# Optimization experiments

Hardware: AMD Instinct MI355X
Metric: run time of the kernel (lower is better)

The kernel has to match this reference:

```python
import jax, jax.numpy as jnp
import numpy as np

NUM_EMBEDDINGS = 1024
EMBEDDING_DIM = 256
COMMITMENT_COST = 0.25


def setup_inputs() -> dict:
    key = jax.random.key(0)
    kz, kc = jax.random.split(key)
    z = jax.random.normal(kz, (32, 32, 32, EMBEDDING_DIM), dtype=jnp.float32)
    # torch init: uniform(-1/K, 1/K)
    codebook = jax.random.uniform(
        kc, (NUM_EMBEDDINGS, EMBEDDING_DIM), dtype=jnp.float32,
        minval=-1.0 / NUM_EMBEDDINGS, maxval=1.0 / NUM_EMBEDDINGS)
    return {"z": z, "codebook": codebook}


def reference(z, codebook):
    K, D = codebook.shape
    zf = z.reshape(-1, D)                                   # [N, D]
    # squared L2 distances via expansion: ||z||^2 + ||e||^2 - 2 z.e
    distances = (jnp.sum(zf * zf, axis=1, keepdims=True)
                 + jnp.sum(codebook * codebook, axis=1)
                 - 2.0 * jnp.matmul(zf, codebook.T))        # [N, K]
    idx = jnp.argmin(distances, axis=1)                     # [N]
    encodings = jax.nn.one_hot(idx, K, dtype=z.dtype)       # [N, K]
    quantized = jnp.matmul(encodings, codebook).reshape(z.shape)
    e_latent_loss = jnp.mean((jax.lax.stop_gradient(quantized) - z) ** 2)
    q_latent_loss = jnp.mean((quantized - jax.lax.stop_gradient(z)) ** 2)
    loss = q_latent_loss + COMMITMENT_COST * e_latent_loss
    quantized_st = z + jax.lax.stop_gradient(quantized - z)  # straight-through
    return quantized_st, loss, encodings
```

## Files before the change

### kernel.cpp

```cpp
#include <hip/hip_runtime.h>

#define N_ROWS 32768
#define DIM 256
#define K_CODES 1024
#define OUT_QUANT 8388608

__device__ __forceinline__ float pw128sq(const float* __restrict__ x) {
  float r[8];
#pragma unroll
  for (int j = 0; j < 8; ++j) r[j] = __fmul_rn(x[j], x[j]);
#pragma unroll
  for (int i = 8; i < 128; i += 8) {
#pragma unroll
    for (int j = 0; j < 8; ++j) r[j] = __fadd_rn(r[j], __fmul_rn(x[i + j], x[i + j]));
  }
  return __fadd_rn(__fadd_rn(__fadd_rn(r[0], r[1]), __fadd_rn(r[2], r[3])),
                   __fadd_rn(__fadd_rn(r[4], r[5]), __fadd_rn(r[6], r[7])));
}

__global__ __launch_bounds__(256) void row_norms(const float* __restrict__ z,
                                                 float* __restrict__ rn) {
  int r = blockIdx.x * 256 + threadIdx.x;
  if (r < N_ROWS)
    rn[r] = __fadd_rn(pw128sq(z + (size_t)r * DIM), pw128sq(z + (size_t)r * DIM + 128));
}

__global__ __launch_bounds__(256) void code_norms(const float* __restrict__ cb,
                                                  float* __restrict__ cn) {
  int k = blockIdx.x * 256 + threadIdx.x;
  if (k < K_CODES)
    cn[k] = __fadd_rn(pw128sq(cb + (size_t)k * DIM), pw128sq(cb + (size_t)k * DIM + 128));
}

__global__ __launch_bounds__(256) void gemm_argmin(
    const float* __restrict__ z, const float* __restrict__ cb,
    const float* __restrict__ rn, const float* __restrict__ cn,
    unsigned long long* __restrict__ keys) {
  __shared__ float As[16][132];
  __shared__ float Bs[16][132];
  __shared__ unsigned long long red[128];

  const int bm = blockIdx.x >> 3;
  const int bn = blockIdx.x & 7;
  const int row0 = bm * 128, col0 = bn * 128;
  const int tid = threadIdx.x;
  const int tx = tid & 15, ty = tid >> 4;
  const int lrow = tid >> 2;
  const int lc4 = (tid & 3) << 2;

  if (tid < 128) red[tid] = ~0ull;

  float acc[8][8];
#pragma unroll
  for (int i = 0; i < 8; ++i)
#pragma unroll
    for (int j = 0; j < 8; ++j) acc[i][j] = 0.f;

  for (int kk = 0; kk < DIM; kk += 16) {
    float4 a0 = *(const float4*)(z + (size_t)(row0 + lrow) * DIM + kk + lc4);
    float4 a1 = *(const float4*)(z + (size_t)(row0 + lrow + 64) * DIM + kk + lc4);
    float4 b0 = *(const float4*)(cb + (size_t)(col0 + lrow) * DIM + kk + lc4);
    float4 b1 = *(const float4*)(cb + (size_t)(col0 + lrow + 64) * DIM + kk + lc4);
    __syncthreads();
    As[lc4 + 0][lrow] = a0.x; As[lc4 + 1][lrow] = a0.y;
    As[lc4 + 2][lrow] = a0.z; As[lc4 + 3][lrow] = a0.w;
    As[lc4 + 0][lrow + 64] = a1.x; As[lc4 + 1][lrow + 64] = a1.y;
    As[lc4 + 2][lrow + 64] = a1.z; As[lc4 + 3][lrow + 64] = a1.w;
    Bs[lc4 + 0][lrow] = b0.x; Bs[lc4 + 1][lrow] = b0.y;
    Bs[lc4 + 2][lrow] = b0.z; Bs[lc4 + 3][lrow] = b0.w;
    Bs[lc4 + 0][lrow + 64] = b1.x; Bs[lc4 + 1][lrow + 64] = b1.y;
    Bs[lc4 + 2][lrow + 64] = b1.z; Bs[lc4 + 3][lrow + 64] = b1.w;
    __syncthreads();
#pragma unroll
    for (int k = 0; k < 16; ++k) {
      float av[8], bv[8];
      *(float4*)&av[0] = *(const float4*)&As[k][ty * 8];
      *(float4*)&av[4] = *(const float4*)&As[k][ty * 8 + 4];
      *(float4*)&bv[0] = *(const float4*)&Bs[k][tx * 4];
      *(float4*)&bv[4] = *(const float4*)&Bs[k][tx * 4 + 64];
#pragma unroll
      for (int i = 0; i < 8; ++i)
#pragma unroll
        for (int j = 0; j < 8; ++j) acc[i][j] = fmaf(av[i], bv[j], acc[i][j]);
    }
  }

#pragma unroll
  for (int i = 0; i < 8; ++i) {
    const int m = ty * 8 + i;
    const float a = rn[row0 + m];
    unsigned long long best = ~0ull;
#pragma unroll
    for (int j = 0; j < 8; ++j) {
      const int c = col0 + ((j < 4) ? (tx * 4 + j) : (64 + tx * 4 + (j - 4)));
      const float d = __fsub_rn(__fadd_rn(a, cn[c]), 2.0f * acc[i][j]);
      unsigned int b = __float_as_uint(d);
      b = (b & 0x80000000u) ? ~b : (b | 0x80000000u);
      const unsigned long long key = ((unsigned long long)b << 32) | (unsigned int)c;
      if (key < best) best = key;
    }
    atomicMin(&red[m], best);
  }
  __syncthreads();
  if (tid < 128) atomicMin(&keys[row0 + tid], red[tid]);
}

__global__ __launch_bounds__(256) void quantize_out(
    const float* __restrict__ z, const float* __restrict__ cb,
    const unsigned long long* __restrict__ keys,
    float* __restrict__ out, float* __restrict__ lossp) {
  __shared__ float ls[4];
  const int wid = threadIdx.x >> 6, lane = threadIdx.x & 63;
  const int row = blockIdx.x * 4 + wid;
  const int idx = (int)(keys[row] & 0xffffffffull);
  const float4 zv = *(const float4*)(z + (size_t)row * DIM + lane * 4);
  const float4 qv = *(const float4*)(cb + (size_t)idx * DIM + lane * 4);
  const float dx = __fsub_rn(qv.x, zv.x);
  const float dy = __fsub_rn(qv.y, zv.y);
  const float dzz = __fsub_rn(qv.z, zv.z);
  const float dw = __fsub_rn(qv.w, zv.w);
  float4 ov;
  ov.x = __fadd_rn(zv.x, dx); ov.y = __fadd_rn(zv.y, dy);
  ov.z = __fadd_rn(zv.z, dzz); ov.w = __fadd_rn(zv.w, dw);
  *(float4*)(out + (size_t)row * DIM + lane * 4) = ov;
  float s = dx * dx + dy * dy + dzz * dzz + dw * dw;
#pragma unroll
  for (int o = 32; o > 0; o >>= 1) s += __shfl_down(s, o);
  if (lane == 0) ls[wid] = s;
  __syncthreads();
  if (threadIdx.x == 0) lossp[blockIdx.x] = ls[0] + ls[1] + ls[2] + ls[3];
  if (lane == 0) out[(size_t)OUT_QUANT + 1 + (size_t)row * K_CODES + idx] = 1.0f;
}

__global__ __launch_bounds__(256) void loss_final(const float* __restrict__ lossp,
                                                  float* __restrict__ out) {
  __shared__ float sm[256];
  float v = 0.f;
  for (int i = threadIdx.x; i < 8192; i += 256) v += lossp[i];
  sm[threadIdx.x] = v;
  __syncthreads();
  for (int s = 128; s > 0; s >>= 1) {
    if (threadIdx.x < s) sm[threadIdx.x] += sm[threadIdx.x + s];
    __syncthreads();
  }
  if (threadIdx.x == 0) out[OUT_QUANT] = sm[0] * (1.25f / 8388608.0f);
}

extern "C" void kernel_launch(void* const* d_in, const int* in_sizes, int n_in,
                              void* d_out, int out_size, void* d_ws, size_t ws_size,
                              hipStream_t stream) {
  const float* z = (const float*)d_in[0];
  const float* cb = (const float*)d_in[1];
  float* out = (float*)d_out;

  unsigned long long* keys = (unsigned long long*)d_ws;
  float* rn = (float*)((char*)d_ws + (size_t)N_ROWS * 8);
  float* cn = rn + N_ROWS;
  float* lossp = cn + K_CODES;

  hipMemsetAsync(out + OUT_QUANT, 0, (size_t)(1 + (size_t)N_ROWS * K_CODES) * sizeof(float), stream);
  hipMemsetAsync(keys, 0xFF, (size_t)N_ROWS * 8, stream);

  row_norms<<<N_ROWS / 256, 256, 0, stream>>>(z, rn);
  code_norms<<<K_CODES / 256, 256, 0, stream>>>(cb, cn);
  gemm_argmin<<<2048, 256, 0, stream>>>(z, cb, rn, cn, keys);
  quantize_out<<<N_ROWS / 4, 256, 0, stream>>>(z, cb, keys, out, lossp);
  loss_final<<<1, 256, 0, stream>>>(lossp, out);
}
```

Measured before the change: 429.3 us.

## Use split-bf16 MFMA for distance GEMM and write one-hot rows directly

```diff
diff --git a/kernel.cpp b/kernel.cpp
--- a/kernel.cpp
+++ b/kernel.cpp
@@ -4,6 +4,10 @@
 #define DIM 256
 #define K_CODES 1024
 #define OUT_QUANT 8388608
+
+typedef unsigned long long ull;
+typedef __attribute__((ext_vector_type(8))) short bf16x8;
+typedef __attribute__((ext_vector_type(4))) float f32x4;
 
 __device__ __forceinline__ float pw128sq(const float* __restrict__ x) {
   float r[8];
@@ -32,83 +36,149 @@
     cn[k] = __fadd_rn(pw128sq(cb + (size_t)k * DIM), pw128sq(cb + (size_t)k * DIM + 128));
 }
 
-__global__ __launch_bounds__(256) void gemm_argmin(
-    const float* __restrict__ z, const float* __restrict__ cb,
+__device__ __forceinline__ void split3(float x, unsigned short& h, unsigned short& m,
+                                       unsigned short& l) {
+  unsigned int u = __float_as_uint(x);
+  unsigned int hb = u & 0xFFFF0000u;
+  h = (unsigned short)(hb >> 16);
+  float r1 = __fsub_rn(x, __uint_as_float(hb));
+  unsigned int mb = __float_as_uint(r1) & 0xFFFF0000u;
+  m = (unsigned short)(mb >> 16);
+  float r2 = __fsub_rn(r1, __uint_as_float(mb));
+  unsigned int u2 = __float_as_uint(r2);
+  unsigned int rounded = u2 + 0x7FFFu + ((u2 >> 16) & 1u);
+  l = (unsigned short)(rounded >> 16);
+}
+
+__global__ __launch_bounds__(256) void split_z(const float* __restrict__ z,
+                                               unsigned short* __restrict__ zh,
+                                               unsigned short* __restrict__ zm,
+                                               unsigned short* __restrict__ zl) {
+  const size_t i = ((size_t)blockIdx.x * 256 + threadIdx.x) * 4;
+  const float4 v = *(const float4*)(z + i);
+  ushort4 h, m, l;
+  split3(v.x, h.x, m.x, l.x);
+  split3(v.y, h.y, m.y, l.y);
+  split3(v.z, h.z, m.z, l.z);
+  split3(v.w, h.w, m.w, l.w);
+  *(ushort4*)(zh + i) = h;
+  *(ushort4*)(zm + i) = m;
+  *(ushort4*)(zl + i) = l;
+}
+
+__device__ __forceinline__ void lds16(const void* g, void* l) {
+  __builtin_amdgcn_global_load_lds(
+      (const __attribute__((address_space(1))) unsigned int*)g,
+      (__attribute__((address_space(3))) unsigned int*)l, 16, 0, 0);
+}
+
+__device__ __forceinline__ ull shflx64(ull v, int m) {
+  int lo = __shfl_xor((int)(v & 0xffffffffull), m);
+  int hi = __shfl_xor((int)(v >> 32), m);
+  return ((ull)(unsigned int)hi << 32) | (unsigned int)lo;
+}
+
+__global__ __launch_bounds__(256) void gemm_argmin_mfma(
+    const unsigned short* __restrict__ zh, const unsigned short* __restrict__ zm,
+    const unsigned short* __restrict__ zl, const unsigned short* __restrict__ ch,
+    const unsigned short* __restrict__ cm, const unsigned short* __restrict__ cl,
     const float* __restrict__ rn, const float* __restrict__ cn,
-    unsigned long long* __restrict__ keys) {
-  __shared__ float As[16][132];
-  __shared__ float Bs[16][132];
-  __shared__ unsigned long long red[128];
-
-  const int bm = blockIdx.x >> 3;
-  const int bn = blockIdx.x & 7;
+    ull* __restrict__ keys) {
+  __shared__ unsigned short As[4 * 128 * 8];
+  __shared__ unsigned short Bs[4 * 128 * 8];
+
+  const int bid = blockIdx.x;
+  const int xcd = bid & 7;
+  const int i = bid >> 3;
+  const int bm = xcd * 32 + (i >> 3);
+  const int bn = i & 7;
   const int row0 = bm * 128, col0 = bn * 128;
+
   const int tid = threadIdx.x;
-  const int tx = tid & 15, ty = tid >> 4;
-  const int lrow = tid >> 2;
-  const int lc4 = (tid & 3) << 2;
-
-  if (tid < 128) red[tid] = ~0ull;
-
-  float acc[8][8];
-#pragma unroll
-  for (int i = 0; i < 8; ++i)
-#pragma unroll
-    for (int j = 0; j < 8; ++j) acc[i][j] = 0.f;
-
-  for (int kk = 0; kk < DIM; kk += 16) {
-    float4 a0 = *(const float4*)(z + (size_t)(row0 + lrow) * DIM + kk + lc4);
-    float4 a1 = *(const float4*)(z + (size_t)(row0 + lrow + 64) * DIM + kk + lc4);
-    float4 b0 = *(const float4*)(cb + (size_t)(col0 + lrow) * DIM + kk + lc4);
-    float4 b1 = *(const float4*)(cb + (size_t)(col0 + lrow + 64) * DIM + kk + lc4);
-    __syncthreads();
-    As[lc4 + 0][lrow] = a0.x; As[lc4 + 1][lrow] = a0.y;
-    As[lc4 + 2][lrow] = a0.z; As[lc4 + 3][lrow] = a0.w;
-    As[lc4 + 0][lrow + 64] = a1.x; As[lc4 + 1][lrow + 64] = a1.y;
-    As[lc4 + 2][lrow + 64] = a1.z; As[lc4 + 3][lrow + 64] = a1.w;
-    Bs[lc4 + 0][lrow] = b0.x; Bs[lc4 + 1][lrow] = b0.y;
-    Bs[lc4 + 2][lrow] = b0.z; Bs[lc4 + 3][lrow] = b0.w;
-    Bs[lc4 + 0][lrow + 64] = b1.x; Bs[lc4 + 1][lrow + 64] = b1.y;
-    Bs[lc4 + 2][lrow + 64] = b1.z; Bs[lc4 + 3][lrow + 64] = b1.w;
-    __syncthreads();
-#pragma unroll
-    for (int k = 0; k < 16; ++k) {
-      float av[8], bv[8];
-      *(float4*)&av[0] = *(const float4*)&As[k][ty * 8];
-      *(float4*)&av[4] = *(const float4*)&As[k][ty * 8 + 4];
-      *(float4*)&bv[0] = *(const float4*)&Bs[k][tx * 4];
-      *(float4*)&bv[4] = *(const float4*)&Bs[k][tx * 4 + 64];
-#pragma unroll
-      for (int i = 0; i < 8; ++i)
-#pragma unroll
-        for (int j = 0; j < 8; ++j) acc[i][j] = fmaf(av[i], bv[j], acc[i][j]);
+  const int wid = tid >> 6, lane = tid & 63;
+  const int wm = wid >> 1, wn = wid & 1;
+  const int lq = lane >> 4, lr = lane & 15;
+  const int srow = tid & 127, shalf = tid >> 7;
+
+  f32x4 acc[4][4];
+#pragma unroll
+  for (int a = 0; a < 4; ++a)
+#pragma unroll
+    for (int b = 0; b < 4; ++b) acc[a][b] = (f32x4){0.f, 0.f, 0.f, 0.f};
+
+  const unsigned short* As_g_row = nullptr;
+
+  auto kpass = [&](const unsigned short* __restrict__ Ag,
+                   const unsigned short* __restrict__ Bg) {
+    for (int kk = 0; kk < DIM; kk += 32) {
+      __syncthreads();
+#pragma unroll
+      for (int is = 0; is < 2; ++is) {
+        lds16(Ag + (size_t)(row0 + srow) * DIM + kk + is * 16 + shalf * 8,
+              (char*)As + is * 4096 + tid * 16);
+        lds16(Bg + (size_t)(col0 + srow) * DIM + kk + is * 16 + shalf * 8,
+              (char*)Bs + is * 4096 + tid * 16);
+      }
+      __syncthreads();
+
+      bf16x8 av[4], bv[4];
+      const bf16x8* As8 = (const bf16x8*)As;
+      const bf16x8* Bs8 = (const bf16x8*)Bs;
+#pragma unroll
+      for (int fm = 0; fm < 4; ++fm) av[fm] = As8[lq * 128 + wm * 64 + fm * 16 + lr];
+#pragma unroll
+      for (int fn = 0; fn < 4; ++fn) bv[fn] = Bs8[lq * 128 + wn * 64 + fn * 16 + lr];
+#pragma unroll
+      for (int fm = 0; fm < 4; ++fm)
+#pragma unroll
+        for (int fn = 0; fn < 4; ++fn)
+          acc[fm][fn] = __builtin_amdgcn_mfma_f32_16x16x32_bf16(av[fm], bv[fn],
+                                                                acc[fm][fn], 0, 0, 0);
     }
-  }
-
-#pragma unroll
-  for (int i = 0; i < 8; ++i) {
-    const int m = ty * 8 + i;
-    const float a = rn[row0 + m];
-    unsigned long long best = ~0ull;
-#pragma unroll
-    for (int j = 0; j < 8; ++j) {
-      const int c = col0 + ((j < 4) ? (tx * 4 + j) : (64 + tx * 4 + (j - 4)));
-      const float d = __fsub_rn(__fadd_rn(a, cn[c]), 2.0f * acc[i][j]);
-      unsigned int b = __float_as_uint(d);
-      b = (b & 0x80000000u) ? ~b : (b | 0x80000000u);
-      const unsigned long long key = ((unsigned long long)b << 32) | (unsigned int)c;
-      if (key < best) best = key;
+  };
+
+  kpass(zh, ch);
+  kpass(zh, cm);
+  kpass(zm, ch);
+  kpass(zh, cl);
+  kpass(zl, ch);
+  kpass(zm, cm);
+  (void)As_g_row;
+
+  float cnv[4];
+#pragma unroll
+  for (int fn = 0; fn < 4; ++fn) cnv[fn] = cn[col0 + wn * 64 + fn * 16 + lr];
+
+#pragma unroll
+  for (int fm = 0; fm < 4; ++fm) {
+#pragma unroll
+    for (int j = 0; j < 4; ++j) {
+      const int rg = row0 + wm * 64 + fm * 16 + lq * 4 + j;
+      const float a_rn = rn[rg];
+      ull best = ~0ull;
+#pragma unroll
+      for (int fn = 0; fn < 4; ++fn) {
+        const int cg = col0 + wn * 64 + fn * 16 + lr;
+        const float d = __fsub_rn(__fadd_rn(a_rn, cnv[fn]), 2.0f * acc[fm][fn][j]);
+        unsigned int b = __float_as_uint(d);
+        b = (b & 0x80000000u) ? ~b : (b | 0x80000000u);
+        const ull key = ((ull)b << 32) | (unsigned int)cg;
+        if (key < best) best = key;
+      }
+#pragma unroll
+      for (int off = 1; off <= 8; off <<= 1) {
+        ull o = shflx64(best, off);
+        if (o < best) best = o;
+      }
+      if (lr == 0) atomicMin(&keys[rg], best);
     }
-    atomicMin(&red[m], best);
-  }
-  __syncthreads();
-  if (tid < 128) atomicMin(&keys[row0 + tid], red[tid]);
+  }
 }
 
 __global__ __launch_bounds__(256) void quantize_out(
     const float* __restrict__ z, const float* __restrict__ cb,
-    const unsigned long long* __restrict__ keys,
-    float* __restrict__ out, float* __restrict__ lossp) {
+    const ull* __restrict__ keys, float* __restrict__ out,
+    float* __restrict__ lossp) {
   __shared__ float ls[4];
   const int wid = threadIdx.x >> 6, lane = threadIdx.x & 63;
   const int row = blockIdx.x * 4 + wid;
@@ -127,9 +197,19 @@
 #pragma unroll
   for (int o = 32; o > 0; o >>= 1) s += __shfl_down(s, o);
   if (lane == 0) ls[wid] = s;
+
+  float4* enc4 = (float4*)(out + (size_t)OUT_QUANT + 1 + (size_t)row * K_CODES);
+  const int target = idx >> 2, comp = idx & 3;
+#pragma unroll
+  for (int i = 0; i < 4; ++i) {
+    const int f4i = lane + 64 * i;
+    float4 v = {0.f, 0.f, 0.f, 0.f};
+    if (f4i == target) ((float*)&v)[comp] = 1.0f;
+    enc4[f4i] = v;
+  }
+
   __syncthreads();
   if (threadIdx.x == 0) lossp[blockIdx.x] = ls[0] + ls[1] + ls[2] + ls[3];
-  if (lane == 0) out[(size_t)OUT_QUANT + 1 + (size_t)row * K_CODES + idx] = 1.0f;
 }
 
 __global__ __launch_bounds__(256) void loss_final(const float* __restrict__ lossp,
@@ -153,17 +233,25 @@
   const float* cb = (const float*)d_in[1];
   float* out = (float*)d_out;
 
-  unsigned long long* keys = (unsigned long long*)d_ws;
-  float* rn = (float*)((char*)d_ws + (size_t)N_ROWS * 8);
-  float* cn = rn + N_ROWS;
-  float* lossp = cn + K_CODES;
-
-  hipMemsetAsync(out + OUT_QUANT, 0, (size_t)(1 + (size_t)N_ROWS * K_CODES) * sizeof(float), stream);
+  char* w = (char*)d_ws;
+  ull* keys = (ull*)w;
+  float* rn = (float*)(w + (256u << 10));
+  float* cn = (float*)(w + (384u << 10));
+  float* lossp = (float*)(w + (388u << 10));
+  unsigned short* zh = (unsigned short*)(w + (1u << 20));
+  unsigned short* zm = (unsigned short*)(w + (17u << 20));
+  unsigned short* zl = (unsigned short*)(w + (33u << 20));
+  unsigned short* ch = (unsigned short*)(w + (49u << 20));
+  unsigned short* cm = (unsigned short*)(w + (49u << 20) + (512u << 10));
+  unsigned short* cl = (unsigned short*)(w + (50u << 20));
+
   hipMemsetAsync(keys, 0xFF, (size_t)N_ROWS * 8, stream);
 
   row_norms<<<N_ROWS / 256, 256, 0, stream>>>(z, rn);
   code_norms<<<K_CODES / 256, 256, 0, stream>>>(cb, cn);
-  gemm_argmin<<<2048, 256, 0, stream>>>(z, cb, rn, cn, keys);
+  split_z<<<(N_ROWS * DIM) / 1024, 256, 0, stream>>>(z, zh, zm, zl);
+  split_z<<<(K_CODES * DIM) / 1024, 256, 0, stream>>>(cb, ch, cm, cl);
+  gemm_argmin_mfma<<<2048, 256, 0, stream>>>(zh, zm, zl, ch, cm, cl, rn, cn, keys);
   quantize_out<<<N_ROWS / 4, 256, 0, stream>>>(z, cb, keys, out, lossp);
   loss_final<<<1, 256, 0, stream>>>(lossp, out);
 }
```

Measured after the change: 472.3 us. 1.1x slower.
